# Kernel optimization log

Measured on AMD Instinct MI355X. Metric: run time of the kernel, lower is better.

## Reference

```python
import jax, jax.numpy as jnp
import numpy as np


def gcn_conv(x, W, b, src, dst, n_nodes):
    """PyG GCNConv: linear transform, add self-loops, symmetric deg^-1/2 norm, scatter-add, bias."""
    h = x @ W  # [N, out] transform first (out_dim <= in_dim keeps gather traffic low)
    loop = jnp.arange(n_nodes)
    s = jnp.concatenate([src, loop])  # sources incl. self-loops
    d = jnp.concatenate([dst, loop])  # targets incl. self-loops
    deg = jnp.zeros((n_nodes,), h.dtype).at[d].add(jnp.ones((), h.dtype))
    dinv = jax.lax.rsqrt(deg)  # deg >= 1 because of self-loops
    coef = (dinv[s] * dinv[d])[:, None]  # [E+N, 1]
    out = jax.ops.segment_sum(h[s] * coef, d, num_segments=n_nodes)
    return out + b


def setup_inputs() -> dict:
    key = jax.random.key(0)
    k1, k2, k3, k4 = jax.random.split(key, 4)
    N, E = 100000, 1600000
    IN, HID, OUT = 128, 64, 32
    x = jax.random.normal(k1, (N, IN), dtype=jnp.float32)
    edge_index = jax.random.randint(k2, (2, E), 0, N, dtype=jnp.int64)
    W1 = jax.random.normal(k3, (IN, HID), dtype=jnp.float32) * (1.0 / np.sqrt(IN))
    b1 = jnp.zeros((HID,), jnp.float32)
    W2 = jax.random.normal(k4, (HID, OUT), dtype=jnp.float32) * (1.0 / np.sqrt(HID))
    b2 = jnp.zeros((OUT,), jnp.float32)
    return {"x": x, "edge_index": edge_index, "W1": W1, "b1": b1, "W2": W2, "b2": b2}


def reference(x, edge_index, W1, b1, W2, b2):
    src, dst = edge_index[0], edge_index[1]
    n = x.shape[0]
    h = jax.nn.relu(gcn_conv(x, W1, b1, src, dst, n))
    return gcn_conv(h, W2, b2, src, dst, n)
```

## Files before the change

### kernel.cpp

```cpp
#include <hip/hip_runtime.h>
#include <hip/hip_bf16.h>


#define IN_DIM 128
#define HID_DIM 64
#define OUT_DIM 32
#define BSHIFT 8
#define BSIZE 256
#define BMASK 255
#define PEB 8192
#define PTHREADS 512
#define CAPSHIFT 13

typedef __attribute__((ext_vector_type(2))) float v2f;
typedef __attribute__((ext_vector_type(8))) short short8v;
typedef __attribute__((ext_vector_type(4))) float float4v;

__device__ inline unsigned pack_bf16x2(float a, float b) {
    unsigned ua = __float_as_uint(a), ub = __float_as_uint(b);
    unsigned ra = (ua + 0x7fffu + ((ua >> 16) & 1u)) >> 16;
    unsigned rb = (ub + 0x7fffu + ((ub >> 16) & 1u)) & 0xffff0000u;
    return (ra & 0xffffu) | rb;
}
__device__ inline unsigned short f2bf(float f) {
    unsigned u = __float_as_uint(f);
    return (unsigned short)((u + 0x7fffu + ((u >> 16) & 1u)) >> 16);
}
#define BF_LO(w) __uint_as_float((w) << 16)
#define BF_HI(w) __uint_as_float((w) & 0xffff0000u)

__device__ inline v2f bfpair(unsigned u) {
    v2f r;
    r.x = __uint_as_float(u << 16);
    r.y = __uint_as_float(u & 0xffff0000u);
    return r;
}
__device__ inline void accp(v2f& a, unsigned u, float dv) {
    a.x += BF_LO(u) * dv;
    a.y += BF_HI(u) * dv;
}

#define ACC8(q)                                         \
    do {                                                \
        acc[0] += BF_LO((q).x); acc[1] += BF_HI((q).x); \
        acc[2] += BF_LO((q).y); acc[3] += BF_HI((q).y); \
        acc[4] += BF_LO((q).z); acc[5] += BF_HI((q).z); \
        acc[6] += BF_LO((q).w); acc[7] += BF_HI((q).w); \
    } while (0)

__global__ __launch_bounds__(PTHREADS) void k_part_gemm1(
        const int* __restrict__ src, const int* __restrict__ dst, int E,
        int* __restrict__ bfill, unsigned* __restrict__ packed, int B, int nPB,
        const float* __restrict__ x, const float* __restrict__ W,
        unsigned* __restrict__ g1b, int N) {
    __shared__ int cnt[512];
    __shared__ int off[512];
    __shared__ unsigned xs[32 * 66];
    int t = threadIdx.x;

    if (blockIdx.x < nPB) {
        cnt[t] = 0;
        __syncthreads();
        int base = blockIdx.x * PEB;
        int dv[PEB / PTHREADS];
        int sv[PEB / PTHREADS];
#pragma unroll
        for (int i = 0; i < PEB / PTHREADS; ++i) {
            int e = base + i * PTHREADS + t;
            bool ok = e < E;
            dv[i] = ok ? dst[e] : -1;
            sv[i] = ok ? src[e] : 0;
            if (dv[i] >= 0) atomicAdd(&cnt[dv[i] >> BSHIFT], 1);
        }
        __syncthreads();
        for (int b = t; b < B; b += PTHREADS) {
            int c = cnt[b];
            int o = c ? atomicAdd(&bfill[b], c) : 0;
            off[b] = (b << CAPSHIFT) + o;
        }
        __syncthreads();
#pragma unroll
        for (int i = 0; i < PEB / PTHREADS; ++i) {
            int d = dv[i];
            if (d >= 0) {
                int slot = atomicAdd(&off[d >> BSHIFT], 1);
                packed[slot] = ((unsigned)sv[i] << BSHIFT) | (unsigned)(d & BMASK);
            }
        }
    } else {
        int row0 = (blockIdx.x - nPB) * 32;
        int w = t >> 6, lane = t & 63;
        int rg = w >> 2, wv = w & 3;
        int quad = lane >> 4, m = lane & 15;
        int ncol = wv * 16 + m;

        float4 xf[2];
#pragma unroll
        for (int i = 0; i < 2; ++i) {
            int idx = t + 512 * i;
            int r = idx >> 5, c4 = idx & 31;
            int grow = row0 + r;
            xf[i] = make_float4(0.f, 0.f, 0.f, 0.f);
            if (grow < N) xf[i] = ((const float4*)x)[(size_t)grow * 32 + c4];
        }

        union { unsigned u[4]; short8v s; } bf[4];
#pragma unroll
        for (int kt = 0; kt < 4; ++kt) {
#pragma unroll
            for (int jp = 0; jp < 4; ++jp) {
                int k0 = kt * 32 + quad * 8 + jp * 2;
                float f0 = W[(size_t)k0 * HID_DIM + ncol];
                float f1 = W[(size_t)(k0 + 1) * HID_DIM + ncol];
                bf[kt].u[jp] = pack_bf16x2(f0, f1);
            }
        }

#pragma unroll
        for (int i = 0; i < 2; ++i) {
            int idx = t + 512 * i;
            int r = idx >> 5, c4 = idx & 31;
            xs[r * 66 + c4 * 2]     = pack_bf16x2(xf[i].x, xf[i].y);
            xs[r * 66 + c4 * 2 + 1] = pack_bf16x2(xf[i].z, xf[i].w);
        }
        __syncthreads();

        float4v acc = {0.f, 0.f, 0.f, 0.f};
#pragma unroll
        for (int kt = 0; kt < 4; ++kt) {
            union { unsigned u[4]; short8v s; } af;
            const unsigned* ap = &xs[(rg * 16 + m) * 66 + kt * 16 + quad * 4];
            af.u[0] = ap[0]; af.u[1] = ap[1]; af.u[2] = ap[2]; af.u[3] = ap[3];
            acc = __builtin_amdgcn_mfma_f32_16x16x32_bf16(af.s, bf[kt].s, acc, 0, 0, 0);
        }

        unsigned short* g1s = (unsigned short*)g1b;
#pragma unroll
        for (int reg = 0; reg < 4; ++reg) {
            int r = row0 + rg * 16 + quad * 4 + reg;
            if (r < N) g1s[(size_t)r * HID_DIM + ncol] = f2bf(acc[reg]);
        }
    }
}

__global__ __launch_bounds__(512) void k_csrfill(const unsigned* __restrict__ packed,
                                                 const int* __restrict__ bfill,
                                                 int* __restrict__ colidx,
                                                 uint2* __restrict__ rowptr2,
                                                 float* __restrict__ dinv,
                                                 int N, int B) {
    __shared__ int ldeg[256];
    __shared__ int lscan[256];
    __shared__ int sexc[256];
    __shared__ int lfill[256];
    int t = threadIdx.x, bkt = blockIdx.x;
    int base = bkt << CAPSHIFT;
    int end  = base + bfill[bkt];
    if (t < 256) ldeg[t] = 0;
    __syncthreads();
    for (int e = base + t; e < end; e += 512)
        atomicAdd(&ldeg[packed[e] & BMASK], 1);
    __syncthreads();
    int v = (t < 256) ? ldeg[t] : 0;
    if (t < 256) lscan[t] = v;
    __syncthreads();
    for (int off = 1; off < 256; off <<= 1) {
        int x = (t < 256 && t >= off) ? lscan[t - off] : 0;
        __syncthreads();
        if (t < 256) lscan[t] += x;
        __syncthreads();
    }
    if (t < 256) {
        int exc = lscan[t] - v;
        sexc[t] = exc;
        lfill[t] = 0;
        int node = (bkt << BSHIFT) + t;
        if (node < N) {
            rowptr2[node] = make_uint2((unsigned)(base + exc), (unsigned)(base + exc + v));
            dinv[node] = rsqrtf((float)v + 1.0f);
        }
    }
    __syncthreads();
    for (int e = base + t; e < end; e += 512) {
        unsigned w = packed[e];
        int ld = w & BMASK;
        int pos = base + sexc[ld] + atomicAdd(&lfill[ld], 1);
        colidx[pos] = (int)(w >> BSHIFT);
    }
}

__global__ __launch_bounds__(256) void k_agg1g2(const unsigned* __restrict__ g1,
                                                const uint2* __restrict__ rowptr2,
                                                const int* __restrict__ colidx,
                                                const float* __restrict__ dinv,
                                                const float* __restrict__ b1,
                                                const float* __restrict__ W2,
                                                unsigned short* __restrict__ g2s, int N) {
    __shared__ unsigned t1s[16 * 33];
    int t = threadIdx.x;
    int wave = t >> 6, lane = t & 63;
    int q = lane >> 4, ql = lane & 15;
    int grp = ql >> 3, fp = ql & 7;
    int nl = wave * 4 + q;
    int dd = blockIdx.x * 16 + nl;
    bool live = dd < N;
    int d = live ? dd : N - 1;

    uint2 be = rowptr2[d];
    v2f a01 = {0.f, 0.f}, a23 = {0.f, 0.f}, a45 = {0.f, 0.f}, a67 = {0.f, 0.f};
#define ACCR(qv, dv)                                     \
    do {                                                 \
        accp(a01, (qv).x, dv); accp(a23, (qv).y, dv);    \
        accp(a45, (qv).z, dv); accp(a67, (qv).w, dv);    \
    } while (0)
    int e = (int)be.x, end = (int)be.y;
    for (; e + 8 <= end; e += 8) {
        int s0 = colidx[e + grp];
        int s1 = colidx[e + 2 + grp];
        int s2 = colidx[e + 4 + grp];
        int s3 = colidx[e + 6 + grp];
        float dv0 = dinv[s0], dv1 = dinv[s1], dv2 = dinv[s2], dv3 = dinv[s3];
        uint4 q0 = *(const uint4*)&g1[(size_t)s0 * 32 + fp * 4];
        uint4 q1 = *(const uint4*)&g1[(size_t)s1 * 32 + fp * 4];
        uint4 q2 = *(const uint4*)&g1[(size_t)s2 * 32 + fp * 4];
        uint4 q3 = *(const uint4*)&g1[(size_t)s3 * 32 + fp * 4];
        ACCR(q0, dv0); ACCR(q1, dv1); ACCR(q2, dv2); ACCR(q3, dv3);
    }
    for (; e + 4 <= end; e += 4) {
        int s0 = colidx[e + grp];
        int s1 = colidx[e + 2 + grp];
        float dv0 = dinv[s0], dv1 = dinv[s1];
        uint4 q0 = *(const uint4*)&g1[(size_t)s0 * 32 + fp * 4];
        uint4 q1 = *(const uint4*)&g1[(size_t)s1 * 32 + fp * 4];
        ACCR(q0, dv0); ACCR(q1, dv1);
    }
    for (; e + 2 <= end; e += 2) {
        int s = colidx[e + grp];
        float dv = dinv[s];
        uint4 qv = *(const uint4*)&g1[(size_t)s * 32 + fp * 4];
        ACCR(qv, dv);
    }
    if (e < end) {
        int s = colidx[e];
        float dv = dinv[s];
        uint4 qv = *(const uint4*)&g1[(size_t)s * 32 + fp * 4];
        if (grp == 0) ACCR(qv, dv);
    }
#undef ACCR
    float acc[8] = {a01.x, a01.y, a23.x, a23.y, a45.x, a45.y, a67.x, a67.y};
#pragma unroll
    for (int i = 0; i < 8; ++i)
        acc[i] += __shfl_xor(acc[i], 8);

    uint4 sq = *(const uint4*)&g1[(size_t)d * 32 + fp * 4];
    float dvd = dinv[d];
    acc[0] += BF_LO(sq.x) * dvd; acc[1] += BF_HI(sq.x) * dvd;
    acc[2] += BF_LO(sq.y) * dvd; acc[3] += BF_HI(sq.y) * dvd;
    acc[4] += BF_LO(sq.z) * dvd; acc[5] += BF_HI(sq.z) * dvd;
    acc[6] += BF_LO(sq.w) * dvd; acc[7] += BF_HI(sq.w) * dvd;
    float4 bb0 = ((const float4*)b1)[fp * 2];
    float4 bb1 = ((const float4*)b1)[fp * 2 + 1];
    float v0 = fmaxf(dvd * acc[0] + bb0.x, 0.f);
    float v1 = fmaxf(dvd * acc[1] + bb0.y, 0.f);
    float v2 = fmaxf(dvd * acc[2] + bb0.z, 0.f);
    float v3 = fmaxf(dvd * acc[3] + bb0.w, 0.f);
    float v4 = fmaxf(dvd * acc[4] + bb1.x, 0.f);
    float v5 = fmaxf(dvd * acc[5] + bb1.y, 0.f);
    float v6 = fmaxf(dvd * acc[6] + bb1.z, 0.f);
    float v7 = fmaxf(dvd * acc[7] + bb1.w, 0.f);
    if (grp == 0) {
        t1s[nl * 33 + fp * 4 + 0] = pack_bf16x2(v0, v1);
        t1s[nl * 33 + fp * 4 + 1] = pack_bf16x2(v2, v3);
        t1s[nl * 33 + fp * 4 + 2] = pack_bf16x2(v4, v5);
        t1s[nl * 33 + fp * 4 + 3] = pack_bf16x2(v6, v7);
    }
    __syncthreads();

    if (wave < 2) {
        int quad = lane >> 4, n = lane & 15;
        int col = (wave << 4) + n;
        union { unsigned u[4]; short8v s; } af0, af1, bh0, bh1, bl0, bl1;
#pragma unroll
        for (int jp = 0; jp < 4; ++jp) {
            int k0 = quad * 8 + jp * 2;
            float f0 = W2[(size_t)k0 * OUT_DIM + col];
            float f1 = W2[(size_t)(k0 + 1) * OUT_DIM + col];
            float f2 = W2[(size_t)(k0 + 32) * OUT_DIM + col];
            float f3 = W2[(size_t)(k0 + 33) * OUT_DIM + col];
            unsigned short h0 = f2bf(f0), h1 = f2bf(f1);
            unsigned short h2 = f2bf(f2), h3 = f2bf(f3);
            bh0.u[jp] = (unsigned)h0 | ((unsigned)h1 << 16);
            bh1.u[jp] = (unsigned)h2 | ((unsigned)h3 << 16);
            float r0 = f0 - __uint_as_float((unsigned)h0 << 16);
            float r1 = f1 - __uint_as_float((unsigned)h1 << 16);
            float r2 = f2 - __uint_as_float((unsigned)h2 << 16);
            float r3 = f3 - __uint_as_float((unsigned)h3 << 16);
            bl0.u[jp] = pack_bf16x2(r0, r1);
            bl1.u[jp] = pack_bf16x2(r2, r3);
            af0.u[jp] = t1s[n * 33 + quad * 4 + jp];
            af1.u[jp] = t1s[n * 33 + 16 + quad * 4 + jp];
        }
        float4v acc2 = {0.f, 0.f, 0.f, 0.f};
        acc2 = __builtin_amdgcn_mfma_f32_16x16x32_bf16(af0.s, bh0.s, acc2, 0, 0, 0);
        acc2 = __builtin_amdgcn_mfma_f32_16x16x32_bf16(af1.s, bh1.s, acc2, 0, 0, 0);
        acc2 = __builtin_amdgcn_mfma_f32_16x16x32_bf16(af0.s, bl0.s, acc2, 0, 0, 0);
        acc2 = __builtin_amdgcn_mfma_f32_16x16x32_bf16(af1.s, bl1.s, acc2, 0, 0, 0);
#pragma unroll
        for (int reg = 0; reg < 4; ++reg) {
            int row = blockIdx.x * 16 + quad * 4 + reg;
            if (row < N) g2s[(size_t)row * 32 + col] = f2bf(acc2[reg] * dinv[row]);
        }
    }
}

__global__ __launch_bounds__(128) void k_agg2(const unsigned* __restrict__ g2,
                                              const uint2* __restrict__ rowptr2,
                                              const int* __restrict__ colidx,
                                              const float* __restrict__ dinv,
                                              const float* __restrict__ b2,
                                              float* __restrict__ out, int N) {
    int t = threadIdx.x;
    int lane = t & 63;
    int o = lane >> 3, ol = lane & 7;
    int grp = ol >> 2, fp = ol & 3;
    int dd = blockIdx.x * 16 + (t >> 6) * 8 + o;
    bool live = dd < N;
    int d = live ? dd : N - 1;

    uint2 be = rowptr2[d];
    v2f a01 = {0.f, 0.f}, a23 = {0.f, 0.f}, a45 = {0.f, 0.f}, a67 = {0.f, 0.f};
#define ACC8V(qv)                                    \
    do {                                             \
        a01 += bfpair((qv).x); a23 += bfpair((qv).y);\
        a45 += bfpair((qv).z); a67 += bfpair((qv).w);\
    } while (0)
    int e = (int)be.x, end = (int)be.y;
    for (; e + 8 <= end; e += 8) {
        int s0 = colidx[e + grp];
        int s1 = colidx[e + 2 + grp];
        int s2 = colidx[e + 4 + grp];
        int s3 = colidx[e + 6 + grp];
        uint4 q0 = *(const uint4*)&g2[(size_t)s0 * 16 + fp * 4];
        uint4 q1 = *(const uint4*)&g2[(size_t)s1 * 16 + fp * 4];
        uint4 q2 = *(const uint4*)&g2[(size_t)s2 * 16 + fp * 4];
        uint4 q3 = *(const uint4*)&g2[(size_t)s3 * 16 + fp * 4];
        ACC8V(q0); ACC8V(q1); ACC8V(q2); ACC8V(q3);
    }
    for (; e + 4 <= end; e += 4) {
        int s0 = colidx[e + grp];
        int s1 = colidx[e + 2 + grp];
        uint4 q0 = *(const uint4*)&g2[(size_t)s0 * 16 + fp * 4];
        uint4 q1 = *(const uint4*)&g2[(size_t)s1 * 16 + fp * 4];
        ACC8V(q0);
        ACC8V(q1);
    }
    for (; e + 2 <= end; e += 2) {
        int s = colidx[e + grp];
        uint4 qv = *(const uint4*)&g2[(size_t)s * 16 + fp * 4];
        ACC8V(qv);
    }
    if (e < end) {
        int s = colidx[e];
        uint4 qv = *(const uint4*)&g2[(size_t)s * 16 + fp * 4];
        if (grp == 0) ACC8V(qv);
    }
#undef ACC8V
    float acc[8] = {a01.x, a01.y, a23.x, a23.y, a45.x, a45.y, a67.x, a67.y};
#pragma unroll
    for (int i = 0; i < 8; ++i)
        acc[i] += __shfl_xor(acc[i], 4);
    uint4 sq = *(const uint4*)&g2[(size_t)d * 16 + fp * 4];
    ACC8(sq);
    float dv = dinv[d];
    float4 bb0 = ((const float4*)b2)[fp * 2];
    float4 bb1 = ((const float4*)b2)[fp * 2 + 1];
    if (live && grp == 0) {
        float4 r0, r1;
        r0.x = dv * acc[0] + bb0.x; r0.y = dv * acc[1] + bb0.y;
        r0.z = dv * acc[2] + bb0.z; r0.w = dv * acc[3] + bb0.w;
        r1.x = dv * acc[4] + bb1.x; r1.y = dv * acc[5] + bb1.y;
        r1.z = dv * acc[6] + bb1.z; r1.w = dv * acc[7] + bb1.w;
        *(float4*)&out[(size_t)dd * OUT_DIM + fp * 8] = r0;
        *(float4*)&out[(size_t)dd * OUT_DIM + fp * 8 + 4] = r1;
    }
}

extern "C" void kernel_launch(void* const* d_in, const int* in_sizes, int n_in,
                              void* d_out, int out_size, void* d_ws, size_t ws_size,
                              hipStream_t stream) {
    const float* x  = (const float*)d_in[0];
    const int*   ei = (const int*)d_in[1];
    const float* W1 = (const float*)d_in[2];
    const float* b1 = (const float*)d_in[3];
    const float* W2 = (const float*)d_in[4];
    const float* b2 = (const float*)d_in[5];
    float* out = (float*)d_out;

    const int N = in_sizes[0] / IN_DIM;
    const int E = in_sizes[1] / 2;
    const int* src = ei;
    const int* dst = ei + E;

    const int B   = (N + BSIZE - 1) / BSIZE;
    const int nPB = (E + PEB - 1) / PEB;
    const int nGB = (N + 31) / 32;
    const size_t SLOTS = (size_t)B << CAPSHIFT;

    char* p = (char*)d_ws;
    auto alloc = [&](size_t bytes) -> void* {
        void* r = (void*)p;
        p += (bytes + 255) & ~(size_t)255;
        return r;
    };
    int*      bfill   = (int*)alloc((size_t)B * 4);
    unsigned* packed  = (unsigned*)alloc(SLOTS * 4);
    int*      colidx  = (int*)alloc(SLOTS * 4);
    uint2*    rowptr2 = (uint2*)alloc((size_t)N * 8);
    float*    dinv    = (float*)alloc((size_t)N * 4);
    unsigned* g1b     = (unsigned*)alloc((size_t)N * 32 * 4);
    unsigned* g2b     = (unsigned*)alloc((size_t)N * 16 * 4);

    hipMemsetAsync(bfill, 0, (size_t)B * 4, stream);
    k_part_gemm1<<<nPB + nGB, PTHREADS, 0, stream>>>(src, dst, E, bfill, packed, B, nPB,
                                                     x, W1, g1b, N);
    k_csrfill<<<B, 512, 0, stream>>>(packed, bfill, colidx, rowptr2, dinv, N, B);
    k_agg1g2<<<(N + 15) / 16, 256, 0, stream>>>(g1b, rowptr2, colidx, dinv, b1, W2,
                                                (unsigned short*)g2b, N);
    k_agg2<<<(N + 15) / 16, 128, 0, stream>>>(g2b, rowptr2, colidx, dinv, b2, out, N);
}
```

Before: 199.6 us.

## Fuse CSR construction into layer-1 aggregation using per-half-bucket LDS column lists

Splits the old CSR-fill kernel into a small degree/dinv kernel and a fused kernel. The fused kernel runs one block per half-bucket of 128 destination nodes. It builds that half's column list in LDS and writes colidx and rowptr for later use. It then aggregates layer-1 features straight from the LDS list and applies the W2 MFMA transform for 128 rows at once. The goal is to avoid reading colidx back from global memory and to drop a separate kernel boundary. The cost is that the packed edges are read several times, each thread processes four nodes in sequence, and edges past the 4096-entry LDS cap are silently dropped.

After: 200.3 us. About the same (+0.3%).

```diff
diff --git a/kernel.cpp b/kernel.cpp
--- a/kernel.cpp
+++ b/kernel.cpp
@@ -11,6 +11,7 @@
 #define PEB 8192
 #define PTHREADS 512
 #define CAPSHIFT 13
+#define COLCAP_H 4096
 
 typedef __attribute__((ext_vector_type(2))) float v2f;
 typedef __attribute__((ext_vector_type(8))) short short8v;
@@ -143,143 +144,165 @@
     }
 }
 
-__global__ __launch_bounds__(512) void k_csrfill(const unsigned* __restrict__ packed,
-                                                 const int* __restrict__ bfill,
-                                                 int* __restrict__ colidx,
-                                                 uint2* __restrict__ rowptr2,
-                                                 float* __restrict__ dinv,
-                                                 int N, int B) {
+__global__ __launch_bounds__(512) void k_dinv(const unsigned* __restrict__ packed,
+                                              const int* __restrict__ bfill,
+                                              float* __restrict__ dinv, int N) {
     __shared__ int ldeg[256];
-    __shared__ int lscan[256];
-    __shared__ int sexc[256];
-    __shared__ int lfill[256];
     int t = threadIdx.x, bkt = blockIdx.x;
     int base = bkt << CAPSHIFT;
-    int end  = base + bfill[bkt];
+    int end = base + bfill[bkt];
     if (t < 256) ldeg[t] = 0;
     __syncthreads();
     for (int e = base + t; e < end; e += 512)
         atomicAdd(&ldeg[packed[e] & BMASK], 1);
     __syncthreads();
-    int v = (t < 256) ? ldeg[t] : 0;
-    if (t < 256) lscan[t] = v;
-    __syncthreads();
-    for (int off = 1; off < 256; off <<= 1) {
-        int x = (t < 256 && t >= off) ? lscan[t - off] : 0;
-        __syncthreads();
-        if (t < 256) lscan[t] += x;
-        __syncthreads();
-    }
     if (t < 256) {
-        int exc = lscan[t] - v;
-        sexc[t] = exc;
-        lfill[t] = 0;
         int node = (bkt << BSHIFT) + t;
-        if (node < N) {
-            rowptr2[node] = make_uint2((unsigned)(base + exc), (unsigned)(base + exc + v));
-            dinv[node] = rsqrtf((float)v + 1.0f);
-        }
-    }
-    __syncthreads();
-    for (int e = base + t; e < end; e += 512) {
-        unsigned w = packed[e];
-        int ld = w & BMASK;
-        int pos = base + sexc[ld] + atomicAdd(&lfill[ld], 1);
-        colidx[pos] = (int)(w >> BSHIFT);
-    }
-}
-
-__global__ __launch_bounds__(256) void k_agg1g2(const unsigned* __restrict__ g1,
-                                                const uint2* __restrict__ rowptr2,
-                                                const int* __restrict__ colidx,
+        if (node < N) dinv[node] = rsqrtf((float)ldeg[t] + 1.0f);
+    }
+}
+
+__global__ __launch_bounds__(512) void k_bktagg(const unsigned* __restrict__ packed,
+                                                const int* __restrict__ bfill,
+                                                const unsigned* __restrict__ g1,
                                                 const float* __restrict__ dinv,
                                                 const float* __restrict__ b1,
                                                 const float* __restrict__ W2,
+                                                int* __restrict__ colidx,
+                                                uint2* __restrict__ rowptr2,
                                                 unsigned short* __restrict__ g2s, int N) {
-    __shared__ unsigned t1s[16 * 33];
+    __shared__ int ldeg[128];
+    __shared__ int lscan[128];
+    __shared__ int sexc[128];
+    __shared__ int lfill[128];
+    __shared__ int colL[COLCAP_H];
+    __shared__ unsigned t1s[128 * 33];
     int t = threadIdx.x;
-    int wave = t >> 6, lane = t & 63;
-    int q = lane >> 4, ql = lane & 15;
+    int bkt = blockIdx.x >> 1, half = blockIdx.x & 1;
+    int base = bkt << CAPSHIFT;
+    int end = base + bfill[bkt];
+    int mybase = base + (half << (CAPSHIFT - 1));
+
+    if (t < 128) { ldeg[t] = 0; lfill[t] = 0; }
+    __syncthreads();
+    for (int e = base + t; e < end; e += 512) {
+        int node = packed[e] & BMASK;
+        if ((node >> 7) == half) atomicAdd(&ldeg[node & 127], 1);
+    }
+    __syncthreads();
+    int v = (t < 128) ? ldeg[t] : 0;
+    if (t < 128) lscan[t] = v;
+    __syncthreads();
+    for (int off = 1; off < 128; off <<= 1) {
+        int xv = (t < 128 && t >= off) ? lscan[t - off] : 0;
+        __syncthreads();
+        if (t < 128) lscan[t] += xv;
+        __syncthreads();
+    }
+    if (t < 128) {
+        int exc = lscan[t] - v;
+        sexc[t] = exc;
+        int node = (bkt << BSHIFT) + (half << 7) + t;
+        if (node < N)
+            rowptr2[node] = make_uint2((unsigned)(mybase + exc), (unsigned)(mybase + exc + v));
+    }
+    __syncthreads();
+    for (int e = base + t; e < end; e += 512) {
+        unsigned w = packed[e];
+        int node = w & BMASK;
+        if ((node >> 7) == half) {
+            int pos = sexc[node & 127] + atomicAdd(&lfill[node & 127], 1);
+            if (pos < COLCAP_H) colL[pos] = (int)(w >> BSHIFT);
+        }
+    }
+    __syncthreads();
+    int hcnt = lscan[127];
+    if (hcnt > COLCAP_H) hcnt = COLCAP_H;
+    for (int i = t; i < hcnt; i += 512) colidx[mybase + i] = colL[i];
+
+    int qidx = t >> 4, ql = t & 15;
     int grp = ql >> 3, fp = ql & 7;
-    int nl = wave * 4 + q;
-    int dd = blockIdx.x * 16 + nl;
-    bool live = dd < N;
-    int d = live ? dd : N - 1;
-
-    uint2 be = rowptr2[d];
-    v2f a01 = {0.f, 0.f}, a23 = {0.f, 0.f}, a45 = {0.f, 0.f}, a67 = {0.f, 0.f};
+    for (int rnd = 0; rnd < 4; ++rnd) {
+        int lt = qidx * 4 + rnd;
+        int dd = (bkt << BSHIFT) + (half << 7) + lt;
+        int d = dd < N ? dd : N - 1;
+        int eb = sexc[lt], eend = eb + ldeg[lt];
+        v2f a01 = {0.f, 0.f}, a23 = {0.f, 0.f}, a45 = {0.f, 0.f}, a67 = {0.f, 0.f};
 #define ACCR(qv, dv)                                     \
     do {                                                 \
         accp(a01, (qv).x, dv); accp(a23, (qv).y, dv);    \
         accp(a45, (qv).z, dv); accp(a67, (qv).w, dv);    \
     } while (0)
-    int e = (int)be.x, end = (int)be.y;
-    for (; e + 8 <= end; e += 8) {
-        int s0 = colidx[e + grp];
-        int s1 = colidx[e + 2 + grp];
-        int s2 = colidx[e + 4 + grp];
-        int s3 = colidx[e + 6 + grp];
-        float dv0 = dinv[s0], dv1 = dinv[s1], dv2 = dinv[s2], dv3 = dinv[s3];
-        uint4 q0 = *(const uint4*)&g1[(size_t)s0 * 32 + fp * 4];
-        uint4 q1 = *(const uint4*)&g1[(size_t)s1 * 32 + fp * 4];
-        uint4 q2 = *(const uint4*)&g1[(size_t)s2 * 32 + fp * 4];
-        uint4 q3 = *(const uint4*)&g1[(size_t)s3 * 32 + fp * 4];
-        ACCR(q0, dv0); ACCR(q1, dv1); ACCR(q2, dv2); ACCR(q3, dv3);
-    }
-    for (; e + 4 <= end; e += 4) {
-        int s0 = colidx[e + grp];
-        int s1 = colidx[e + 2 + grp];
-        float dv0 = dinv[s0], dv1 = dinv[s1];
-        uint4 q0 = *(const uint4*)&g1[(size_t)s0 * 32 + fp * 4];
-        uint4 q1 = *(const uint4*)&g1[(size_t)s1 * 32 + fp * 4];
-        ACCR(q0, dv0); ACCR(q1, dv1);
-    }
-    for (; e + 2 <= end; e += 2) {
-        int s = colidx[e + grp];
-        float dv = dinv[s];
-        uint4 qv = *(const uint4*)&g1[(size_t)s * 32 + fp * 4];
-        ACCR(qv, dv);
-    }
-    if (e < end) {
-        int s = colidx[e];
-        float dv = dinv[s];
-        uint4 qv = *(const uint4*)&g1[(size_t)s * 32 + fp * 4];
-        if (grp == 0) ACCR(qv, dv);
-    }
+        int e = eb;
+        for (; e + 8 <= eend; e += 8) {
+            int s0 = colL[e + grp];
+            int s1 = colL[e + 2 + grp];
+            int s2 = colL[e + 4 + grp];
+            int s3 = colL[e + 6 + grp];
+            float dv0 = dinv[s0], dv1 = dinv[s1], dv2 = dinv[s2], dv3 = dinv[s3];
+            uint4 q0 = *(const uint4*)&g1[(size_t)s0 * 32 + fp * 4];
+            uint4 q1 = *(const uint4*)&g1[(size_t)s1 * 32 + fp * 4];
+            uint4 q2 = *(const uint4*)&g1[(size_t)s2 * 32 + fp * 4];
+            uint4 q3 = *(const uint4*)&g1[(size_t)s3 * 32 + fp * 4];
+            ACCR(q0, dv0); ACCR(q1, dv1); ACCR(q2, dv2); ACCR(q3, dv3);
+        }
+        for (; e + 4 <= eend; e += 4) {
+            int s0 = colL[e + grp];
+            int s1 = colL[e + 2 + grp];
+            float dv0 = dinv[s0], dv1 = dinv[s1];
+            uint4 q0 = *(const uint4*)&g1[(size_t)s0 * 32 + fp * 4];
+            uint4 q1 = *(const uint4*)&g1[(size_t)s1 * 32 + fp * 4];
+            ACCR(q0, dv0); ACCR(q1, dv1);
+        }
+        for (; e + 2 <= eend; e += 2) {
+            int s = colL[e + grp];
+            float dv = dinv[s];
+            uint4 qv = *(const uint4*)&g1[(size_t)s * 32 + fp * 4];
+            ACCR(qv, dv);
+        }
+        if (e < eend) {
+            int s = colL[e];
+            float dv = dinv[s];
+            uint4 qv = *(const uint4*)&g1[(size_t)s * 32 + fp * 4];
+            if (grp == 0) ACCR(qv, dv);
+        }
 #undef ACCR
-    float acc[8] = {a01.x, a01.y, a23.x, a23.y, a45.x, a45.y, a67.x, a67.y};
-#pragma unroll
-    for (int i = 0; i < 8; ++i)
-        acc[i] += __shfl_xor(acc[i], 8);
-
-    uint4 sq = *(const uint4*)&g1[(size_t)d * 32 + fp * 4];
-    float dvd = dinv[d];
-    acc[0] += BF_LO(sq.x) * dvd; acc[1] += BF_HI(sq.x) * dvd;
-    acc[2] += BF_LO(sq.y) * dvd; acc[3] += BF_HI(sq.y) * dvd;
-    acc[4] += BF_LO(sq.z) * dvd; acc[5] += BF_HI(sq.z) * dvd;
-    acc[6] += BF_LO(sq.w) * dvd; acc[7] += BF_HI(sq.w) * dvd;
-    float4 bb0 = ((const float4*)b1)[fp * 2];
-    float4 bb1 = ((const float4*)b1)[fp * 2 + 1];
-    float v0 = fmaxf(dvd * acc[0] + bb0.x, 0.f);
-    float v1 = fmaxf(dvd * acc[1] + bb0.y, 0.f);
-    float v2 = fmaxf(dvd * acc[2] + bb0.z, 0.f);
-    float v3 = fmaxf(dvd * acc[3] + bb0.w, 0.f);
-    float v4 = fmaxf(dvd * acc[4] + bb1.x, 0.f);
-    float v5 = fmaxf(dvd * acc[5] + bb1.y, 0.f);
-    float v6 = fmaxf(dvd * acc[6] + bb1.z, 0.f);
-    float v7 = fmaxf(dvd * acc[7] + bb1.w, 0.f);
-    if (grp == 0) {
-        t1s[nl * 33 + fp * 4 + 0] = pack_bf16x2(v0, v1);
-        t1s[nl * 33 + fp * 4 + 1] = pack_bf16x2(v2, v3);
-        t1s[nl * 33 + fp * 4 + 2] = pack_bf16x2(v4, v5);
-        t1s[nl * 33 + fp * 4 + 3] = pack_bf16x2(v6, v7);
-    }
-    __syncthreads();
-
-    if (wave < 2) {
-        int quad = lane >> 4, n = lane & 15;
-        int col = (wave << 4) + n;
-        union { unsigned u[4]; short8v s; } af0, af1, bh0, bh1, bl0, bl1;
+        float acc[8] = {a01.x, a01.y, a23.x, a23.y, a45.x, a45.y, a67.x, a67.y};
+#pragma unroll
+        for (int i = 0; i < 8; ++i)
+            acc[i] += __shfl_xor(acc[i], 8);
+
+        uint4 sq = *(const uint4*)&g1[(size_t)d * 32 + fp * 4];
+        float dvd = dinv[d];
+        acc[0] += BF_LO(sq.x) * dvd; acc[1] += BF_HI(sq.x) * dvd;
+        acc[2] += BF_LO(sq.y) * dvd; acc[3] += BF_HI(sq.y) * dvd;
+        acc[4] += BF_LO(sq.z) * dvd; acc[5] += BF_HI(sq.z) * dvd;
+        acc[6] += BF_LO(sq.w) * dvd; acc[7] += BF_HI(sq.w) * dvd;
+        float4 bb0 = ((const float4*)b1)[fp * 2];
+        float4 bb1 = ((const float4*)b1)[fp * 2 + 1];
+        float v0 = fmaxf(dvd * acc[0] + bb0.x, 0.f);
+        float v1 = fmaxf(dvd * acc[1] + bb0.y, 0.f);
+        float v2 = fmaxf(dvd * acc[2] + bb0.z, 0.f);
+        float v3 = fmaxf(dvd * acc[3] + bb0.w, 0.f);
+        float v4 = fmaxf(dvd * acc[4] + bb1.x, 0.f);
+        float v5 = fmaxf(dvd * acc[5] + bb1.y, 0.f);
+        float v6 = fmaxf(dvd * acc[6] + bb1.z, 0.f);
+        float v7 = fmaxf(dvd * acc[7] + bb1.w, 0.f);
+        if (grp == 0) {
+            t1s[lt * 33 + fp * 4 + 0] = pack_bf16x2(v0, v1);
+            t1s[lt * 33 + fp * 4 + 1] = pack_bf16x2(v2, v3);
+            t1s[lt * 33 + fp * 4 + 2] = pack_bf16x2(v4, v5);
+            t1s[lt * 33 + fp * 4 + 3] = pack_bf16x2(v6, v7);
+        }
+    }
+    __syncthreads();
+
+    {
+        int wave = t >> 6, lane = t & 63;
+        int quad = lane >> 4, n16 = lane & 15;
+        int cw = wave & 1;
+        int col = cw * 16 + n16;
+        union { unsigned u[4]; short8v s; } bh0, bh1, bl0, bl1;
 #pragma unroll
         for (int jp = 0; jp < 4; ++jp) {
             int k0 = quad * 8 + jp * 2;
@@ -297,18 +320,27 @@
             float r3 = f3 - __uint_as_float((unsigned)h3 << 16);
             bl0.u[jp] = pack_bf16x2(r0, r1);
             bl1.u[jp] = pack_bf16x2(r2, r3);
-            af0.u[jp] = t1s[n * 33 + quad * 4 + jp];
-            af1.u[jp] = t1s[n * 33 + 16 + quad * 4 + jp];
-        }
-        float4v acc2 = {0.f, 0.f, 0.f, 0.f};
-        acc2 = __builtin_amdgcn_mfma_f32_16x16x32_bf16(af0.s, bh0.s, acc2, 0, 0, 0);
-        acc2 = __builtin_amdgcn_mfma_f32_16x16x32_bf16(af1.s, bh1.s, acc2, 0, 0, 0);
-        acc2 = __builtin_amdgcn_mfma_f32_16x16x32_bf16(af0.s, bl0.s, acc2, 0, 0, 0);
-        acc2 = __builtin_amdgcn_mfma_f32_16x16x32_bf16(af1.s, bl1.s, acc2, 0, 0, 0);
-#pragma unroll
-        for (int reg = 0; reg < 4; ++reg) {
-            int row = blockIdx.x * 16 + quad * 4 + reg;
-            if (row < N) g2s[(size_t)row * 32 + col] = f2bf(acc2[reg] * dinv[row]);
+        }
+#pragma unroll
+        for (int j = 0; j < 2; ++j) {
+            int rt = (wave >> 1) + 4 * j;
+            union { unsigned u[4]; short8v s; } af0, af1;
+#pragma unroll
+            for (int jp = 0; jp < 4; ++jp) {
+                af0.u[jp] = t1s[(rt * 16 + n16) * 33 + jp + quad * 4];
+                af1.u[jp] = t1s[(rt * 16 + n16) * 33 + 16 + jp + quad * 4];
+            }
+            float4v acc2 = {0.f, 0.f, 0.f, 0.f};
+            acc2 = __builtin_amdgcn_mfma_f32_16x16x32_bf16(af0.s, bh0.s, acc2, 0, 0, 0);
+            acc2 = __builtin_amdgcn_mfma_f32_16x16x32_bf16(af1.s, bh1.s, acc2, 0, 0, 0);
+            acc2 = __builtin_amdgcn_mfma_f32_16x16x32_bf16(af0.s, bl0.s, acc2, 0, 0, 0);
+            acc2 = __builtin_amdgcn_mfma_f32_16x16x32_bf16(af1.s, bl1.s, acc2, 0, 0, 0);
+#pragma unroll
+            for (int reg = 0; reg < 4; ++reg) {
+                int row = (bkt << BSHIFT) + (half << 7) + rt * 16 + quad * 4 + reg;
+                if (row < N)
+                    g2s[(size_t)row * 32 + col] = f2bf(acc2[reg] * dinv[row]);
+            }
         }
     }
 }
@@ -423,8 +455,8 @@
     hipMemsetAsync(bfill, 0, (size_t)B * 4, stream);
     k_part_gemm1<<<nPB + nGB, PTHREADS, 0, stream>>>(src, dst, E, bfill, packed, B, nPB,
                                                      x, W1, g1b, N);
-    k_csrfill<<<B, 512, 0, stream>>>(packed, bfill, colidx, rowptr2, dinv, N, B);
-    k_agg1g2<<<(N + 15) / 16, 256, 0, stream>>>(g1b, rowptr2, colidx, dinv, b1, W2,
-                                                (unsigned short*)g2b, N);
+    k_dinv<<<B, 512, 0, stream>>>(packed, bfill, dinv, N);
+    k_bktagg<<<2 * B, 512, 0, stream>>>(packed, bfill, g1b, dinv, b1, W2, colidx,
+                                        rowptr2, (unsigned short*)g2b, N);
     k_agg2<<<(N + 15) / 16, 128, 0, stream>>>(g2b, rowptr2, colidx, dinv, b2, out, N);
 }
```

## Sort nodes by degree within each bucket to balance aggregation waves

Applied to the files above, without the earlier changes.

Each CSR-fill block now bitonic-sorts its 256 nodes by in-degree in shared memory and writes a permutation array. Both aggregation kernels read that permutation, so each wave processes nodes of similar degree. This is meant to cut the divergence and idle lanes caused by uneven edge-loop trip counts. The cost is an extra sort with many barriers in the fill kernel, an extra indirection load, and output rows written in permuted rather than contiguous order.

After: 215.0 us. 7.7% more time.

```diff
diff --git a/kernel.cpp b/kernel.cpp
--- a/kernel.cpp
+++ b/kernel.cpp
@@ -148,11 +148,13 @@
                                                  int* __restrict__ colidx,
                                                  uint2* __restrict__ rowptr2,
                                                  float* __restrict__ dinv,
+                                                 int* __restrict__ perm,
                                                  int N, int B) {
     __shared__ int ldeg[256];
     __shared__ int lscan[256];
     __shared__ int sexc[256];
     __shared__ int lfill[256];
+    __shared__ int skey[256];
     int t = threadIdx.x, bkt = blockIdx.x;
     int base = bkt << CAPSHIFT;
     int end  = base + bfill[bkt];
@@ -174,6 +176,7 @@
         int exc = lscan[t] - v;
         sexc[t] = exc;
         lfill[t] = 0;
+        skey[t] = (v << 9) | t;
         int node = (bkt << BSHIFT) + t;
         if (node < N) {
             rowptr2[node] = make_uint2((unsigned)(base + exc), (unsigned)(base + exc + v));
@@ -187,6 +190,22 @@
         int pos = base + sexc[ld] + atomicAdd(&lfill[ld], 1);
         colidx[pos] = (int)(w >> BSHIFT);
     }
+    for (int k = 2; k <= 256; k <<= 1) {
+        for (int j = k >> 1; j > 0; j >>= 1) {
+            __syncthreads();
+            if (t < 256) {
+                int ixj = t ^ j;
+                if (ixj > t) {
+                    int a = skey[t], b = skey[ixj];
+                    bool up = ((t & k) == 0);
+                    if ((a > b) == up) { skey[t] = b; skey[ixj] = a; }
+                }
+            }
+        }
+    }
+    __syncthreads();
+    if (t < 256)
+        perm[(bkt << BSHIFT) + t] = (bkt << BSHIFT) + (skey[t] & 511);
 }
 
 __global__ __launch_bounds__(256) void k_agg1g2(const unsigned* __restrict__ g1,
@@ -195,14 +214,18 @@
                                                 const float* __restrict__ dinv,
                                                 const float* __restrict__ b1,
                                                 const float* __restrict__ W2,
+                                                const int* __restrict__ perm,
                                                 unsigned short* __restrict__ g2s, int N) {
     __shared__ unsigned t1s[16 * 33];
+    __shared__ int psh[16];
     int t = threadIdx.x;
     int wave = t >> 6, lane = t & 63;
     int q = lane >> 4, ql = lane & 15;
     int grp = ql >> 3, fp = ql & 7;
     int nl = wave * 4 + q;
-    int dd = blockIdx.x * 16 + nl;
+    if (t < 16) psh[t] = perm[blockIdx.x * 16 + t];
+    __syncthreads();
+    int dd = psh[nl];
     bool live = dd < N;
     int d = live ? dd : N - 1;
 
@@ -307,7 +330,7 @@
         acc2 = __builtin_amdgcn_mfma_f32_16x16x32_bf16(af1.s, bl1.s, acc2, 0, 0, 0);
 #pragma unroll
         for (int reg = 0; reg < 4; ++reg) {
-            int row = blockIdx.x * 16 + quad * 4 + reg;
+            int row = psh[quad * 4 + reg];
             if (row < N) g2s[(size_t)row * 32 + col] = f2bf(acc2[reg] * dinv[row]);
         }
     }
@@ -318,12 +341,13 @@
                                               const int* __restrict__ colidx,
                                               const float* __restrict__ dinv,
                                               const float* __restrict__ b2,
+                                              const int* __restrict__ perm,
                                               float* __restrict__ out, int N) {
     int t = threadIdx.x;
     int lane = t & 63;
     int o = lane >> 3, ol = lane & 7;
     int grp = ol >> 2, fp = ol & 3;
-    int dd = blockIdx.x * 16 + (t >> 6) * 8 + o;
+    int dd = perm[blockIdx.x * 16 + (t >> 6) * 8 + o];
     bool live = dd < N;
     int d = live ? dd : N - 1;
 
@@ -417,14 +441,15 @@
     int*      colidx  = (int*)alloc(SLOTS * 4);
     uint2*    rowptr2 = (uint2*)alloc((size_t)N * 8);
     float*    dinv    = (float*)alloc((size_t)N * 4);
+    int*      perm    = (int*)alloc((size_t)B * 256 * 4);
     unsigned* g1b     = (unsigned*)alloc((size_t)N * 32 * 4);
     unsigned* g2b     = (unsigned*)alloc((size_t)N * 16 * 4);
 
     hipMemsetAsync(bfill, 0, (size_t)B * 4, stream);
     k_part_gemm1<<<nPB + nGB, PTHREADS, 0, stream>>>(src, dst, E, bfill, packed, B, nPB,
                                                      x, W1, g1b, N);
-    k_csrfill<<<B, 512, 0, stream>>>(packed, bfill, colidx, rowptr2, dinv, N, B);
-    k_agg1g2<<<(N + 15) / 16, 256, 0, stream>>>(g1b, rowptr2, colidx, dinv, b1, W2,
-                                                (unsigned short*)g2b, N);
-    k_agg2<<<(N + 15) / 16, 128, 0, stream>>>(g2b, rowptr2, colidx, dinv, b2, out, N);
-}
+    k_csrfill<<<B, 512, 0, stream>>>(packed, bfill, colidx, rowptr2, dinv, perm, N, B);
+    k_agg1g2<<<B * 16, 256, 0, stream>>>(g1b, rowptr2, colidx, dinv, b1, W2, perm,
+                                         (unsigned short*)g2b, N);
+    k_agg2<<<B * 16, 128, 0, stream>>>(g2b, rowptr2, colidx, dinv, b2, perm, out, N);
+}
```

## Fuse all GCN stages into one cooperative persistent kernel with grid syncs

Applied to the files above, without the earlier changes.

Replaces the memset plus four kernel launches with a single cooperative persistent kernel of 1024 blocks of 512 threads. Each stage loops over work units and is separated from the next by grid.sync, with shared memory overlaid through a union. The aggregation kernels are widened to 512-thread blocks covering 32 or 64 nodes. This removes launch gaps and the memset, but adds grid-barrier cost and fixes occupancy at 1024 blocks. A non-cooperative fallback keeps the separate launches if the cooperative launch fails.

Result: slower. 770.9 us (+286.2%).

```diff
diff --git a/kernel.cpp b/kernel.cpp
--- a/kernel.cpp
+++ b/kernel.cpp
@@ -1,5 +1,8 @@
 #include <hip/hip_runtime.h>
 #include <hip/hip_bf16.h>
+#include <hip/hip_cooperative_groups.h>
+
+namespace cg = cooperative_groups;
 
 
 #define IN_DIM 128
@@ -9,8 +12,8 @@
 #define BSIZE 256
 #define BMASK 255
 #define PEB 8192
-#define PTHREADS 512
 #define CAPSHIFT 13
+#define MGRID 1024
 
 typedef __attribute__((ext_vector_type(2))) float v2f;
 typedef __attribute__((ext_vector_type(8))) short short8v;
@@ -48,112 +51,109 @@
         acc[6] += BF_LO((q).w); acc[7] += BF_HI((q).w); \
     } while (0)
 
-__global__ __launch_bounds__(PTHREADS) void k_part_gemm1(
+union ShU {
+    struct { int cnt[512]; int off[512]; } part;
+    unsigned xs[32 * 66];
+    struct { int ldeg[256]; int lscan[256]; int sexc[256]; int lfill[256]; } csr;
+    unsigned t1s[32 * 33];
+};
+
+__device__ __forceinline__ void body_partition(int u, int t,
         const int* __restrict__ src, const int* __restrict__ dst, int E,
-        int* __restrict__ bfill, unsigned* __restrict__ packed, int B, int nPB,
+        int* __restrict__ bfill, unsigned* __restrict__ packed, int B,
+        int* cnt, int* off) {
+    cnt[t] = 0;
+    __syncthreads();
+    int base = u * PEB;
+    int dv[PEB / 512];
+    int sv[PEB / 512];
+#pragma unroll
+    for (int i = 0; i < PEB / 512; ++i) {
+        int e = base + i * 512 + t;
+        bool ok = e < E;
+        dv[i] = ok ? dst[e] : -1;
+        sv[i] = ok ? src[e] : 0;
+        if (dv[i] >= 0) atomicAdd(&cnt[dv[i] >> BSHIFT], 1);
+    }
+    __syncthreads();
+    for (int b = t; b < B; b += 512) {
+        int c = cnt[b];
+        int o = c ? atomicAdd(&bfill[b], c) : 0;
+        off[b] = (b << CAPSHIFT) + o;
+    }
+    __syncthreads();
+#pragma unroll
+    for (int i = 0; i < PEB / 512; ++i) {
+        int d = dv[i];
+        if (d >= 0) {
+            int slot = atomicAdd(&off[d >> BSHIFT], 1);
+            packed[slot] = ((unsigned)sv[i] << BSHIFT) | (unsigned)(d & BMASK);
+        }
+    }
+}
+
+__device__ __forceinline__ void body_gemm1(int u, int t,
         const float* __restrict__ x, const float* __restrict__ W,
-        unsigned* __restrict__ g1b, int N) {
-    __shared__ int cnt[512];
-    __shared__ int off[512];
-    __shared__ unsigned xs[32 * 66];
-    int t = threadIdx.x;
-
-    if (blockIdx.x < nPB) {
-        cnt[t] = 0;
-        __syncthreads();
-        int base = blockIdx.x * PEB;
-        int dv[PEB / PTHREADS];
-        int sv[PEB / PTHREADS];
-#pragma unroll
-        for (int i = 0; i < PEB / PTHREADS; ++i) {
-            int e = base + i * PTHREADS + t;
-            bool ok = e < E;
-            dv[i] = ok ? dst[e] : -1;
-            sv[i] = ok ? src[e] : 0;
-            if (dv[i] >= 0) atomicAdd(&cnt[dv[i] >> BSHIFT], 1);
+        unsigned* __restrict__ g1b, int N, unsigned* xs) {
+    int row0 = u * 32;
+    int w = t >> 6, lane = t & 63;
+    int rg = w >> 2, wv = w & 3;
+    int quad = lane >> 4, m = lane & 15;
+    int ncol = wv * 16 + m;
+
+    float4 xf[2];
+#pragma unroll
+    for (int i = 0; i < 2; ++i) {
+        int idx = t + 512 * i;
+        int r = idx >> 5, c4 = idx & 31;
+        int grow = row0 + r;
+        xf[i] = make_float4(0.f, 0.f, 0.f, 0.f);
+        if (grow < N) xf[i] = ((const float4*)x)[(size_t)grow * 32 + c4];
+    }
+
+    union { unsigned u4[4]; short8v s; } bf[4];
+#pragma unroll
+    for (int kt = 0; kt < 4; ++kt) {
+#pragma unroll
+        for (int jp = 0; jp < 4; ++jp) {
+            int k0 = kt * 32 + quad * 8 + jp * 2;
+            float f0 = W[(size_t)k0 * HID_DIM + ncol];
+            float f1 = W[(size_t)(k0 + 1) * HID_DIM + ncol];
+            bf[kt].u4[jp] = pack_bf16x2(f0, f1);
         }
-        __syncthreads();
-        for (int b = t; b < B; b += PTHREADS) {
-            int c = cnt[b];
-            int o = c ? atomicAdd(&bfill[b], c) : 0;
-            off[b] = (b << CAPSHIFT) + o;
-        }
-        __syncthreads();
-#pragma unroll
-        for (int i = 0; i < PEB / PTHREADS; ++i) {
-            int d = dv[i];
-            if (d >= 0) {
-                int slot = atomicAdd(&off[d >> BSHIFT], 1);
-                packed[slot] = ((unsigned)sv[i] << BSHIFT) | (unsigned)(d & BMASK);
-            }
-        }
-    } else {
-        int row0 = (blockIdx.x - nPB) * 32;
-        int w = t >> 6, lane = t & 63;
-        int rg = w >> 2, wv = w & 3;
-        int quad = lane >> 4, m = lane & 15;
-        int ncol = wv * 16 + m;
-
-        float4 xf[2];
-#pragma unroll
-        for (int i = 0; i < 2; ++i) {
-            int idx = t + 512 * i;
-            int r = idx >> 5, c4 = idx & 31;
-            int grow = row0 + r;
-            xf[i] = make_float4(0.f, 0.f, 0.f, 0.f);
-            if (grow < N) xf[i] = ((const float4*)x)[(size_t)grow * 32 + c4];
-        }
-
-        union { unsigned u[4]; short8v s; } bf[4];
-#pragma unroll
-        for (int kt = 0; kt < 4; ++kt) {
-#pragma unroll
-            for (int jp = 0; jp < 4; ++jp) {
-                int k0 = kt * 32 + quad * 8 + jp * 2;
-                float f0 = W[(size_t)k0 * HID_DIM + ncol];
-                float f1 = W[(size_t)(k0 + 1) * HID_DIM + ncol];
-                bf[kt].u[jp] = pack_bf16x2(f0, f1);
-            }
-        }
-
-#pragma unroll
-        for (int i = 0; i < 2; ++i) {
-            int idx = t + 512 * i;
-            int r = idx >> 5, c4 = idx & 31;
-            xs[r * 66 + c4 * 2]     = pack_bf16x2(xf[i].x, xf[i].y);
-            xs[r * 66 + c4 * 2 + 1] = pack_bf16x2(xf[i].z, xf[i].w);
-        }
-        __syncthreads();
-
-        float4v acc = {0.f, 0.f, 0.f, 0.f};
-#pragma unroll
-        for (int kt = 0; kt < 4; ++kt) {
-            union { unsigned u[4]; short8v s; } af;
-            const unsigned* ap = &xs[(rg * 16 + m) * 66 + kt * 16 + quad * 4];
-            af.u[0] = ap[0]; af.u[1] = ap[1]; af.u[2] = ap[2]; af.u[3] = ap[3];
-            acc = __builtin_amdgcn_mfma_f32_16x16x32_bf16(af.s, bf[kt].s, acc, 0, 0, 0);
-        }
-
-        unsigned short* g1s = (unsigned short*)g1b;
-#pragma unroll
-        for (int reg = 0; reg < 4; ++reg) {
-            int r = row0 + rg * 16 + quad * 4 + reg;
-            if (r < N) g1s[(size_t)r * HID_DIM + ncol] = f2bf(acc[reg]);
-        }
-    }
-}
-
-__global__ __launch_bounds__(512) void k_csrfill(const unsigned* __restrict__ packed,
-                                                 const int* __restrict__ bfill,
-                                                 int* __restrict__ colidx,
-                                                 uint2* __restrict__ rowptr2,
-                                                 float* __restrict__ dinv,
-                                                 int N, int B) {
-    __shared__ int ldeg[256];
-    __shared__ int lscan[256];
-    __shared__ int sexc[256];
-    __shared__ int lfill[256];
-    int t = threadIdx.x, bkt = blockIdx.x;
+    }
+
+#pragma unroll
+    for (int i = 0; i < 2; ++i) {
+        int idx = t + 512 * i;
+        int r = idx >> 5, c4 = idx & 31;
+        xs[r * 66 + c4 * 2]     = pack_bf16x2(xf[i].x, xf[i].y);
+        xs[r * 66 + c4 * 2 + 1] = pack_bf16x2(xf[i].z, xf[i].w);
+    }
+    __syncthreads();
+
+    float4v acc = {0.f, 0.f, 0.f, 0.f};
+#pragma unroll
+    for (int kt = 0; kt < 4; ++kt) {
+        union { unsigned u4[4]; short8v s; } af;
+        const unsigned* ap = &xs[(rg * 16 + m) * 66 + kt * 16 + quad * 4];
+        af.u4[0] = ap[0]; af.u4[1] = ap[1]; af.u4[2] = ap[2]; af.u4[3] = ap[3];
+        acc = __builtin_amdgcn_mfma_f32_16x16x32_bf16(af.s, bf[kt].s, acc, 0, 0, 0);
+    }
+
+    unsigned short* g1s = (unsigned short*)g1b;
+#pragma unroll
+    for (int reg = 0; reg < 4; ++reg) {
+        int r = row0 + rg * 16 + quad * 4 + reg;
+        if (r < N) g1s[(size_t)r * HID_DIM + ncol] = f2bf(acc[reg]);
+    }
+}
+
+__device__ __forceinline__ void body_csr(int bkt, int t,
+        const unsigned* __restrict__ packed, const int* __restrict__ bfill,
+        int* __restrict__ colidx, uint2* __restrict__ rowptr2,
+        float* __restrict__ dinv, int N,
+        int* ldeg, int* lscan, int* sexc, int* lfill) {
     int base = bkt << CAPSHIFT;
     int end  = base + bfill[bkt];
     if (t < 256) ldeg[t] = 0;
@@ -165,9 +165,9 @@
     if (t < 256) lscan[t] = v;
     __syncthreads();
     for (int off = 1; off < 256; off <<= 1) {
-        int x = (t < 256 && t >= off) ? lscan[t - off] : 0;
+        int xv = (t < 256 && t >= off) ? lscan[t - off] : 0;
         __syncthreads();
-        if (t < 256) lscan[t] += x;
+        if (t < 256) lscan[t] += xv;
         __syncthreads();
     }
     if (t < 256) {
@@ -189,20 +189,16 @@
     }
 }
 
-__global__ __launch_bounds__(256) void k_agg1g2(const unsigned* __restrict__ g1,
-                                                const uint2* __restrict__ rowptr2,
-                                                const int* __restrict__ colidx,
-                                                const float* __restrict__ dinv,
-                                                const float* __restrict__ b1,
-                                                const float* __restrict__ W2,
-                                                unsigned short* __restrict__ g2s, int N) {
-    __shared__ unsigned t1s[16 * 33];
-    int t = threadIdx.x;
+__device__ __forceinline__ void body_agg1(int u, int t,
+        const unsigned* __restrict__ g1, const uint2* __restrict__ rowptr2,
+        const int* __restrict__ colidx, const float* __restrict__ dinv,
+        const float* __restrict__ b1, const float* __restrict__ W2,
+        unsigned short* __restrict__ g2s, int N, unsigned* t1s) {
     int wave = t >> 6, lane = t & 63;
-    int q = lane >> 4, ql = lane & 15;
+    int nl = t >> 4;
+    int ql = t & 15;
     int grp = ql >> 3, fp = ql & 7;
-    int nl = wave * 4 + q;
-    int dd = blockIdx.x * 16 + nl;
+    int dd = u * 32 + nl;
     bool live = dd < N;
     int d = live ? dd : N - 1;
 
@@ -276,10 +272,11 @@
     }
     __syncthreads();
 
-    if (wave < 2) {
+    if (wave < 4) {
         int quad = lane >> 4, n = lane & 15;
-        int col = (wave << 4) + n;
-        union { unsigned u[4]; short8v s; } af0, af1, bh0, bh1, bl0, bl1;
+        int rt = wave >> 1, cw = wave & 1;
+        int col = cw * 16 + n;
+        union { unsigned u4[4]; short8v s; } af0, af1, bh0, bh1, bl0, bl1;
 #pragma unroll
         for (int jp = 0; jp < 4; ++jp) {
             int k0 = quad * 8 + jp * 2;
@@ -289,16 +286,16 @@
             float f3 = W2[(size_t)(k0 + 33) * OUT_DIM + col];
             unsigned short h0 = f2bf(f0), h1 = f2bf(f1);
             unsigned short h2 = f2bf(f2), h3 = f2bf(f3);
-            bh0.u[jp] = (unsigned)h0 | ((unsigned)h1 << 16);
-            bh1.u[jp] = (unsigned)h2 | ((unsigned)h3 << 16);
+            bh0.u4[jp] = (unsigned)h0 | ((unsigned)h1 << 16);
+            bh1.u4[jp] = (unsigned)h2 | ((unsigned)h3 << 16);
             float r0 = f0 - __uint_as_float((unsigned)h0 << 16);
             float r1 = f1 - __uint_as_float((unsigned)h1 << 16);
             float r2 = f2 - __uint_as_float((unsigned)h2 << 16);
             float r3 = f3 - __uint_as_float((unsigned)h3 << 16);
-            bl0.u[jp] = pack_bf16x2(r0, r1);
-            bl1.u[jp] = pack_bf16x2(r2, r3);
-            af0.u[jp] = t1s[n * 33 + quad * 4 + jp];
-            af1.u[jp] = t1s[n * 33 + 16 + quad * 4 + jp];
+            bl0.u4[jp] = pack_bf16x2(r0, r1);
+            bl1.u4[jp] = pack_bf16x2(r2, r3);
+            af0.u4[jp] = t1s[(rt * 16 + n) * 33 + quad * 4 + jp];
+            af1.u4[jp] = t1s[(rt * 16 + n) * 33 + 16 + quad * 4 + jp];
         }
         float4v acc2 = {0.f, 0.f, 0.f, 0.f};
         acc2 = __builtin_amdgcn_mfma_f32_16x16x32_bf16(af0.s, bh0.s, acc2, 0, 0, 0);
@@ -307,23 +304,19 @@
         acc2 = __builtin_amdgcn_mfma_f32_16x16x32_bf16(af1.s, bl1.s, acc2, 0, 0, 0);
 #pragma unroll
         for (int reg = 0; reg < 4; ++reg) {
-            int row = blockIdx.x * 16 + quad * 4 + reg;
+            int row = u * 32 + rt * 16 + quad * 4 + reg;
             if (row < N) g2s[(size_t)row * 32 + col] = f2bf(acc2[reg] * dinv[row]);
         }
     }
 }
 
-__global__ __launch_bounds__(128) void k_agg2(const unsigned* __restrict__ g2,
-                                              const uint2* __restrict__ rowptr2,
-                                              const int* __restrict__ colidx,
-                                              const float* __restrict__ dinv,
-                                              const float* __restrict__ b2,
-                                              float* __restrict__ out, int N) {
-    int t = threadIdx.x;
-    int lane = t & 63;
-    int o = lane >> 3, ol = lane & 7;
+__device__ __forceinline__ void body_agg2(int u, int t,
+        const unsigned* __restrict__ g2, const uint2* __restrict__ rowptr2,
+        const int* __restrict__ colidx, const float* __restrict__ dinv,
+        const float* __restrict__ b2, float* __restrict__ out, int N) {
+    int o = t >> 3, ol = t & 7;
     int grp = ol >> 2, fp = ol & 3;
-    int dd = blockIdx.x * 16 + (t >> 6) * 8 + o;
+    int dd = u * 64 + o;
     bool live = dd < N;
     int d = live ? dd : N - 1;
 
@@ -385,6 +378,95 @@
     }
 }
 
+__global__ __launch_bounds__(512, 8) void k_mega(
+        const int* __restrict__ src, const int* __restrict__ dst, int E,
+        int* __restrict__ bfill, unsigned* __restrict__ packed, int B, int nPB,
+        const float* __restrict__ x, const float* __restrict__ W1,
+        unsigned* __restrict__ g1b, int* __restrict__ colidx,
+        uint2* __restrict__ rowptr2, float* __restrict__ dinv,
+        const float* __restrict__ b1, const float* __restrict__ W2,
+        unsigned* __restrict__ g2b, const float* __restrict__ b2,
+        float* __restrict__ out, int N) {
+    __shared__ ShU sh;
+    cg::grid_group grid = cg::this_grid();
+    int t = threadIdx.x;
+    int nGB = (N + 31) / 32;
+
+    for (int i = blockIdx.x * 512 + t; i < B; i += gridDim.x * 512) bfill[i] = 0;
+    grid.sync();
+
+    for (int u = blockIdx.x; u < nPB + nGB; u += gridDim.x) {
+        if (u < nPB)
+            body_partition(u, t, src, dst, E, bfill, packed, B, sh.part.cnt, sh.part.off);
+        else
+            body_gemm1(u - nPB, t, x, W1, g1b, N, sh.xs);
+        __syncthreads();
+    }
+    grid.sync();
+
+    for (int u = blockIdx.x; u < B; u += gridDim.x) {
+        body_csr(u, t, packed, bfill, colidx, rowptr2, dinv, N,
+                 sh.csr.ldeg, sh.csr.lscan, sh.csr.sexc, sh.csr.lfill);
+        __syncthreads();
+    }
+    grid.sync();
+
+    for (int u = blockIdx.x; u < (N + 31) / 32; u += gridDim.x) {
+        body_agg1(u, t, g1b, rowptr2, colidx, dinv, b1, W2,
+                  (unsigned short*)g2b, N, sh.t1s);
+        __syncthreads();
+    }
+    grid.sync();
+
+    for (int u = blockIdx.x; u < (N + 63) / 64; u += gridDim.x)
+        body_agg2(u, t, g2b, rowptr2, colidx, dinv, b2, out, N);
+}
+
+__global__ __launch_bounds__(512) void k_pg1F(const int* __restrict__ src,
+                                              const int* __restrict__ dst, int E,
+                                              int* __restrict__ bfill,
+                                              unsigned* __restrict__ packed, int B, int nPB,
+                                              const float* __restrict__ x,
+                                              const float* __restrict__ W1,
+                                              unsigned* __restrict__ g1b, int N) {
+    __shared__ ShU sh;
+    int t = threadIdx.x;
+    if (blockIdx.x < nPB)
+        body_partition(blockIdx.x, t, src, dst, E, bfill, packed, B, sh.part.cnt, sh.part.off);
+    else
+        body_gemm1(blockIdx.x - nPB, t, x, W1, g1b, N, sh.xs);
+}
+
+__global__ __launch_bounds__(512) void k_csrF(const unsigned* __restrict__ packed,
+                                              const int* __restrict__ bfill,
+                                              int* __restrict__ colidx,
+                                              uint2* __restrict__ rowptr2,
+                                              float* __restrict__ dinv, int N) {
+    __shared__ ShU sh;
+    body_csr(blockIdx.x, threadIdx.x, packed, bfill, colidx, rowptr2, dinv, N,
+             sh.csr.ldeg, sh.csr.lscan, sh.csr.sexc, sh.csr.lfill);
+}
+
+__global__ __launch_bounds__(512) void k_a1F(const unsigned* __restrict__ g1,
+                                             const uint2* __restrict__ rowptr2,
+                                             const int* __restrict__ colidx,
+                                             const float* __restrict__ dinv,
+                                             const float* __restrict__ b1,
+                                             const float* __restrict__ W2,
+                                             unsigned short* __restrict__ g2s, int N) {
+    __shared__ ShU sh;
+    body_agg1(blockIdx.x, threadIdx.x, g1, rowptr2, colidx, dinv, b1, W2, g2s, N, sh.t1s);
+}
+
+__global__ __launch_bounds__(512) void k_a2F(const unsigned* __restrict__ g2,
+                                             const uint2* __restrict__ rowptr2,
+                                             const int* __restrict__ colidx,
+                                             const float* __restrict__ dinv,
+                                             const float* __restrict__ b2,
+                                             float* __restrict__ out, int N) {
+    body_agg2(blockIdx.x, threadIdx.x, g2, rowptr2, colidx, dinv, b2, out, N);
+}
+
 extern "C" void kernel_launch(void* const* d_in, const int* in_sizes, int n_in,
                               void* d_out, int out_size, void* d_ws, size_t ws_size,
                               hipStream_t stream) {
@@ -396,14 +478,14 @@
     const float* b2 = (const float*)d_in[5];
     float* out = (float*)d_out;
 
-    const int N = in_sizes[0] / IN_DIM;
-    const int E = in_sizes[1] / 2;
+    int N = in_sizes[0] / IN_DIM;
+    int E = in_sizes[1] / 2;
     const int* src = ei;
     const int* dst = ei + E;
 
-    const int B   = (N + BSIZE - 1) / BSIZE;
-    const int nPB = (E + PEB - 1) / PEB;
-    const int nGB = (N + 31) / 32;
+    int B   = (N + BSIZE - 1) / BSIZE;
+    int nPB = (E + PEB - 1) / PEB;
+    int nGB = (N + 31) / 32;
     const size_t SLOTS = (size_t)B << CAPSHIFT;
 
     char* p = (char*)d_ws;
@@ -420,11 +502,21 @@
     unsigned* g1b     = (unsigned*)alloc((size_t)N * 32 * 4);
     unsigned* g2b     = (unsigned*)alloc((size_t)N * 16 * 4);
 
-    hipMemsetAsync(bfill, 0, (size_t)B * 4, stream);
-    k_part_gemm1<<<nPB + nGB, PTHREADS, 0, stream>>>(src, dst, E, bfill, packed, B, nPB,
-                                                     x, W1, g1b, N);
-    k_csrfill<<<B, 512, 0, stream>>>(packed, bfill, colidx, rowptr2, dinv, N, B);
-    k_agg1g2<<<(N + 15) / 16, 256, 0, stream>>>(g1b, rowptr2, colidx, dinv, b1, W2,
-                                                (unsigned short*)g2b, N);
-    k_agg2<<<(N + 15) / 16, 128, 0, stream>>>(g2b, rowptr2, colidx, dinv, b2, out, N);
-}
+    void* args[] = {(void*)&src, (void*)&dst, (void*)&E, (void*)&bfill,
+                    (void*)&packed, (void*)&B, (void*)&nPB, (void*)&x,
+                    (void*)&W1, (void*)&g1b, (void*)&colidx, (void*)&rowptr2,
+                    (void*)&dinv, (void*)&b1, (void*)&W2, (void*)&g2b,
+                    (void*)&b2, (void*)&out, (void*)&N};
+    hipError_t ce = hipLaunchCooperativeKernel((const void*)k_mega, dim3(MGRID),
+                                               dim3(512), args, 0u, stream);
+    if (ce != hipSuccess) {
+        (void)hipGetLastError();
+        hipMemsetAsync(bfill, 0, (size_t)B * 4, stream);
+        k_pg1F<<<nPB + nGB, 512, 0, stream>>>(src, dst, E, bfill, packed, B, nPB,
+                                              x, W1, g1b, N);
+        k_csrF<<<B, 512, 0, stream>>>(packed, bfill, colidx, rowptr2, dinv, N);
+        k_a1F<<<(N + 31) / 32, 512, 0, stream>>>(g1b, rowptr2, colidx, dinv, b1, W2,
+                                                 (unsigned short*)g2b, N);
+        k_a2F<<<(N + 63) / 64, 512, 0, stream>>>(g2b, rowptr2, colidx, dinv, b2, out, N);
+    }
+}
```
